# Kernel tuning notes

Hardware: AMD Instinct MI355X
Metric: run time of the kernel (lower is better)

## Reference

```python
import jax, jax.numpy as jnp
import numpy as np

# ---- fixed problem dims (match init_kwargs) ----
B = 256            # graph pairs
NQ, NC = 96, 120   # nodes per query / corpus graph
EQ, EC = 192, 240  # edges per query / corpus graph
M = 256            # max_edge_set_size (pad target)
RAW = 32           # raw node/edge feature dim
H = 64             # node_state_dim
MSG = 128          # message_dim == encoded edge dim
SDIM = 64          # sinkhorn_feature_dim
PROP_STEPS = 3
TIME_STEPS = 2
SINK_ITERS = 10
TEMP = 0.1
N_NODES = B * (NQ + NC)
N_EDGES = B * (EQ + EC)


def _mlp2(x, W1, b1, W2, b2):
    return jax.nn.relu(x @ W1 + b1) @ W2 + b2


def _split_and_stack(ef):
    # edges laid out [q0, c0, q1, c1, ...]; pad each graph's edges to M
    D = ef.shape[-1]
    ef = ef.reshape(B, EQ + EC, D)
    q = jnp.pad(ef[:, :EQ], ((0, 0), (0, M - EQ), (0, 0)))
    c = jnp.pad(ef[:, EQ:], ((0, 0), (0, M - EC), (0, 0)))
    return q, c


def _sinkhorn(log_alpha):
    la = log_alpha / TEMP
    for _ in range(SINK_ITERS):
        la = la - jax.nn.logsumexp(la, axis=2, keepdims=True)
        la = la - jax.nn.logsumexp(la, axis=1, keepdims=True)
    return jnp.exp(la)


def setup_inputs() -> dict:
    key = jax.random.key(0)
    ks = jax.random.split(key, 16)
    rng = np.random.default_rng(0)
    nodes_per_graph = np.tile(np.array([NQ, NC]), B)            # [2B]
    node_offsets = np.concatenate([[0], np.cumsum(nodes_per_graph)[:-1]])
    edges_per_graph = np.tile(np.array([EQ, EC]), B)
    eg = np.repeat(np.arange(2 * B), edges_per_graph)           # graph id per edge
    from_idx = node_offsets[eg] + rng.integers(0, nodes_per_graph[eg])
    to_idx = node_offsets[eg] + rng.integers(0, nodes_per_graph[eg])

    def lin(k, i, o):
        return (jax.random.normal(k, (i, o), jnp.float32) / np.sqrt(i)).astype(jnp.float32)

    return {
        "node_features": jax.random.normal(ks[0], (N_NODES, RAW), jnp.float32),
        "edge_features": jax.random.normal(ks[1], (N_EDGES, RAW), jnp.float32),
        "from_idx": jnp.asarray(from_idx, jnp.int32),
        "to_idx": jnp.asarray(to_idx, jnp.int32),
        "enc_node_W": lin(ks[2], RAW, H), "enc_node_b": jnp.zeros((H,), jnp.float32),
        "enc_edge_W": lin(ks[3], RAW, MSG), "enc_edge_b": jnp.zeros((MSG,), jnp.float32),
        "msg_W1": lin(ks[4], 2 * H + MSG, 2 * MSG), "msg_b1": jnp.zeros((2 * MSG,), jnp.float32),
        "msg_W2": lin(ks[5], 2 * MSG, MSG), "msg_b2": jnp.zeros((MSG,), jnp.float32),
        "upd_W1": lin(ks[6], H + 2 * MSG, 2 * H), "upd_b1": jnp.zeros((2 * H,), jnp.float32),
        "upd_W2": lin(ks[7], 2 * H, H), "upd_b2": jnp.zeros((H,), jnp.float32),
        "int_W1": lin(ks[8], 2 * MSG, 2 * MSG), "int_b1": jnp.zeros((2 * MSG,), jnp.float32),
        "int_W2": lin(ks[9], 2 * MSG, MSG), "int_b2": jnp.zeros((MSG,), jnp.float32),
        "sink_W1": lin(ks[10], MSG, SDIM), "sink_b1": jnp.zeros((SDIM,), jnp.float32),
        "sink_W2": lin(ks[11], SDIM, SDIM), "sink_b2": jnp.zeros((SDIM,), jnp.float32),
    }


def _forward(node_features, edge_features,
             enc_node_W, enc_node_b, enc_edge_W, enc_edge_b,
             msg_W1, msg_b1, msg_W2, msg_b2,
             upd_W1, upd_b1, upd_W2, upd_b2,
             int_W1, int_b1, int_W2, int_b2,
             sink_W1, sink_b1, sink_W2, sink_b2,
             from_idx, to_idx):
    h0 = node_features @ enc_node_W + enc_node_b      # GraphEncoder (nodes)
    e0 = edge_features @ enc_edge_W + enc_edge_b      # GraphEncoder (edges) -> MSG dim
    mask_q = (jnp.arange(M) < EQ).astype(h0.dtype)[None, :, None]
    mask_c = (jnp.arange(M) < EC).astype(h0.dtype)[None, :, None]

    def edge_msgs(h, comb):
        hf, ht = h[from_idx], h[to_idx]
        mf = _mlp2(jnp.concatenate([hf, ht, comb], -1), msg_W1, msg_b1, msg_W2, msg_b2)
        mb = _mlp2(jnp.concatenate([ht, hf, comb], -1), msg_W1, msg_b1, msg_W2, msg_b2)
        return mf, mb

    plan = None
    q_store = c_store = None
    for _ in range(TIME_STEPS):
        h, e = h0, e0
        inter = jnp.zeros((N_EDGES, MSG), e0.dtype)
        for _ in range(PROP_STEPS):
            # interaction encoder on [edge_features_enc, interaction_features]
            comb = _mlp2(jnp.concatenate([e, inter], -1), int_W1, int_b1, int_W2, int_b2)
            # prop_layer: bidirectional messages + aggregation + node update
            mf, mb = edge_msgs(h, comb)
            agg_f = jax.ops.segment_sum(mf, to_idx, num_segments=N_NODES)
            agg_b = jax.ops.segment_sum(mb, from_idx, num_segments=N_NODES)
            h = _mlp2(jnp.concatenate([h, agg_f, agg_b], -1), upd_W1, upd_b1, upd_W2, upd_b2)
            # propagation_messages: per-edge messages from updated node states
            mf2, mb2 = edge_msgs(h, comb)
            e = mf2 + mb2
            # interaction features via transport-plan gather (zeros on first time step)
            if plan is None:
                inter = jnp.zeros((N_EDGES, MSG), e.dtype)
            else:
                qs, cs = _split_and_stack(e)
                q_int = jnp.einsum('bqc,bcd->bqd', plan, cs)[:, :EQ]
                c_int = jnp.einsum('bqc,bqd->bcd', plan, qs)[:, :EC]
                inter = jnp.concatenate([q_int, c_int], 1).reshape(N_EDGES, MSG)
        q_store, c_store = _split_and_stack(e)
        fq = _mlp2(q_store, sink_W1, sink_b1, sink_W2, sink_b2) * mask_q
        fc = _mlp2(c_store, sink_W1, sink_b1, sink_W2, sink_b2) * mask_c
        plan = _sinkhorn(jnp.einsum('bqd,bcd->bqc', fq, fc))
    # feature_alignment_score: -||Q - P C||_1 per pair
    return -jnp.abs(q_store - jnp.einsum('bqc,bcd->bqd', plan, c_store)).sum((1, 2))


def reference(node_features, edge_features, from_idx, to_idx,
              enc_node_W, enc_node_b, enc_edge_W, enc_edge_b,
              msg_W1, msg_b1, msg_W2, msg_b2,
              upd_W1, upd_b1, upd_W2, upd_b2,
              int_W1, int_b1, int_W2, int_b2,
              sink_W1, sink_b1, sink_W2, sink_b2):
    return _forward(node_features, edge_features,
                    enc_node_W, enc_node_b, enc_edge_W, enc_edge_b,
                    msg_W1, msg_b1, msg_W2, msg_b2,
                    upd_W1, upd_b1, upd_W2, upd_b2,
                    int_W1, int_b1, int_W2, int_b2,
                    sink_W1, sink_b1, sink_W2, sink_b2,
                    from_idx, to_idx)
```

## Files before the change

### kernel.cpp

```cpp
#include <hip/hip_runtime.h>
#include <math.h>

constexpr int BATCH = 256;
constexpr int EQ_   = 192;
constexpr int EC_   = 240;
constexpr int EPG   = 432;
constexpr int NPG   = 216;
constexpr int NN    = BATCH * NPG;
constexpr int NE    = BATCH * EPG;

typedef __attribute__((ext_vector_type(8))) short short8;
typedef __attribute__((ext_vector_type(4))) float floatx4;
typedef unsigned short u16;

__device__ __forceinline__ u16 f2bf(float x) {
  union { float f; unsigned u; } c; c.f = x;
  const unsigned r = (c.u + 0x7FFFu + ((c.u >> 16) & 1u)) >> 16;
  return (u16)r;
}
__device__ __forceinline__ float bf2f(u16 x) {
  union { unsigned u; float f; } c; c.u = ((unsigned)x) << 16;
  return c.f;
}
__device__ __forceinline__ unsigned pack2(float a, float b) {
  return (unsigned)f2bf(a) | ((unsigned)f2bf(b) << 16);
}
__device__ __forceinline__ short8 cvt8(const float* __restrict__ p) {
  const float4 a = *(const float4*)p;
  const float4 b = *(const float4*)(p + 4);
  short8 o;
  o[0]=(short)f2bf(a.x); o[1]=(short)f2bf(a.y); o[2]=(short)f2bf(a.z); o[3]=(short)f2bf(a.w);
  o[4]=(short)f2bf(b.x); o[5]=(short)f2bf(b.y); o[6]=(short)f2bf(b.z); o[7]=(short)f2bf(b.w);
  return o;
}

__device__ __forceinline__ void lse_online(float& m, float& s, float tt) {
  if (tt > m) { s = s * __expf(m - tt) + 1.f; m = tt; }
  else        { s += __expf(tt - m); }
}

__global__ __launch_bounds__(256)
void wconv(const float* __restrict__ W, u16* __restrict__ out, int K, int N)
{
  const int i = blockIdx.x * 256 + threadIdx.x;
  if (i < K * N) {
    const int n = i / K, k = i - n * K;
    out[i] = f2bf(W[(size_t)k * N + n]);
  }
}

template<int K1, int HID, int NOUT, int IN_MODE, int DUAL, int OUT_MODE, int WAVES>
__global__ __launch_bounds__(WAVES * 64, 4)
void mlp_mfma(const void* __restrict__ X, const void* __restrict__ P2,
              const void* __restrict__ P3, const u16* __restrict__ CB,
              const int* __restrict__ IA, const int* __restrict__ IB,
              const u16* __restrict__ W1t, const float* __restrict__ B1,
              const u16* __restrict__ W2t, const float* __restrict__ B2,
              float* __restrict__ Yf, u16* __restrict__ Yb0, u16* __restrict__ Yb1)
{
  constexpr int RT  = 32;
  constexpr int THREADS = WAVES * 64;
  constexpr int KCH = K1 / 8;
  constexpr int NT1 = HID / (WAVES * 16);
  constexpr int NT2 = (NOUT / (WAVES * 16) > 0) ? NOUT / (WAVES * 16) : 1;
  constexpr int SAB = RT * K1 * 2;
  constexpr int SHB = RT * (HID + 8) * 2;
  __shared__ __align__(16) char smem[(SAB > SHB ? SAB : SHB)];
  u16* sA = (u16*)smem;
  u16* sH = (u16*)smem;

  const int tid = threadIdx.x;
  const int rowBase = blockIdx.x * RT;

  for (int ch = tid; ch < RT * KCH; ch += THREADS) {
    const int r = ch / KCH, kc = ch - r * KCH;
    const int gr = rowBase + r, k0 = kc * 8;
    short8 pk;
    if constexpr (IN_MODE == 4) {
      const float* Xf  = (const float*)X;
      const float* P2f = (const float*)P2;
      if (k0 < 128)      pk = cvt8(&Xf[(size_t)gr * 128 + k0]);
      else if (P2f)      pk = cvt8(&P2f[(size_t)gr * 128 + (k0 - 128)]);
      else { pk = short8{0,0,0,0,0,0,0,0}; }
    } else if constexpr (IN_MODE == 1) {
      const u16* Hb = (const u16*)X;
      if (k0 < 64)       pk = *(const short8*)&Hb[(size_t)IA[gr] * 64 + k0];
      else if (k0 < 128) pk = *(const short8*)&Hb[(size_t)IB[gr] * 64 + (k0 - 64)];
      else               pk = *(const short8*)&CB[(size_t)gr * 128 + (k0 - 128)];
    } else {
      const u16* Hb = (const u16*)X;
      const u16* A0 = (const u16*)P2;
      const u16* A1 = (const u16*)P3;
      if (k0 < 64)       pk = *(const short8*)&Hb[(size_t)gr * 64 + k0];
      else if (k0 < 192) pk = *(const short8*)&A0[(size_t)gr * 128 + (k0 - 64)];
      else               pk = *(const short8*)&A1[(size_t)gr * 128 + (k0 - 192)];
    }
    const int byte = ((r * K1 + k0) * 2) ^ ((r & 7) << 4);
    *(short8*)((char*)sA + byte) = pk;
  }
  __syncthreads();

  const int wid = tid >> 6, lane = tid & 63;
  const int l15 = lane & 15, lg = lane >> 4;

  floatx4 acc1[1 + DUAL][2][NT1];
  #pragma unroll
  for (int d = 0; d <= DUAL; ++d)
    #pragma unroll
    for (int m = 0; m < 2; ++m)
      #pragma unroll
      for (int n = 0; n < NT1; ++n) acc1[d][m][n] = floatx4{0.f,0.f,0.f,0.f};

  #pragma unroll 2
  for (int kk = 0; kk < K1 / 32; ++kk) {
    short8 bw[NT1];
    #pragma unroll
    for (int n = 0; n < NT1; ++n) {
      const int col = wid * (HID / WAVES) + n * 16 + l15;
      bw[n] = *(const short8*)&W1t[(size_t)col * K1 + kk * 32 + lg * 8];
    }
    #pragma unroll
    for (int d = 0; d <= DUAL; ++d) {
      int k0 = kk * 32 + lg * 8;
      if (DUAL && d && k0 < 128) k0 ^= 64;
      #pragma unroll
      for (int m = 0; m < 2; ++m) {
        const int r = m * 16 + l15;
        const int byte = ((r * K1 + k0) * 2) ^ ((r & 7) << 4);
        const short8 af = *(const short8*)((char*)sA + byte);
        #pragma unroll
        for (int n = 0; n < NT1; ++n)
          acc1[d][m][n] = __builtin_amdgcn_mfma_f32_16x16x32_bf16(af, bw[n], acc1[d][m][n], 0, 0, 0);
      }
    }
  }
  __syncthreads();

  floatx4 accO[2][NT2];
  #pragma unroll
  for (int m = 0; m < 2; ++m)
    #pragma unroll
    for (int n = 0; n < NT2; ++n) accO[m][n] = floatx4{0.f,0.f,0.f,0.f};

  #pragma unroll
  for (int d = 0; d <= DUAL; ++d) {
    #pragma unroll
    for (int n = 0; n < NT1; ++n) {
      const int col = wid * (HID / WAVES) + n * 16 + l15;
      const float b1 = B1[col];
      #pragma unroll
      for (int m = 0; m < 2; ++m)
        #pragma unroll
        for (int r = 0; r < 4; ++r) {
          const int row = m * 16 + lg * 4 + r;
          const float y = acc1[d][m][n][r] + b1;
          sH[row * (HID + 8) + col] = f2bf(y > 0.f ? y : 0.f);
        }
    }
    __syncthreads();
    if (OUT_MODE == 2 && d == 1) {
      #pragma unroll
      for (int m = 0; m < 2; ++m)
        #pragma unroll
        for (int n = 0; n < NT2; ++n) accO[m][n] = floatx4{0.f,0.f,0.f,0.f};
    }
    #pragma unroll 2
    for (int kk = 0; kk < HID / 32; ++kk) {
      short8 bw2[NT2];
      #pragma unroll
      for (int n = 0; n < NT2; ++n) {
        const int col = wid * (NOUT / WAVES) + n * 16 + l15;
        bw2[n] = *(const short8*)&W2t[(size_t)col * HID + kk * 32 + lg * 8];
      }
      #pragma unroll
      for (int m = 0; m < 2; ++m) {
        const short8 af = *(const short8*)&sH[(m * 16 + l15) * (HID + 8) + kk * 32 + lg * 8];
        #pragma unroll
        for (int n = 0; n < NT2; ++n)
          accO[m][n] = __builtin_amdgcn_mfma_f32_16x16x32_bf16(af, bw2[n], accO[m][n], 0, 0, 0);
      }
    }
    if constexpr (OUT_MODE == 2) {
      u16* Y = d ? Yb1 : Yb0;
      #pragma unroll
      for (int n = 0; n < NT2; ++n) {
        const int col = wid * (NOUT / WAVES) + n * 16 + l15;
        const float b2 = B2[col];
        #pragma unroll
        for (int m = 0; m < 2; ++m)
          #pragma unroll
          for (int r = 0; r < 4; ++r) {
            const int gr = rowBase + m * 16 + lg * 4 + r;
            Y[(size_t)gr * NOUT + col] = f2bf(accO[m][n][r] + b2);
          }
      }
    }
    if (DUAL && d == 0) __syncthreads();
  }

  if constexpr (OUT_MODE != 2) {
    #pragma unroll
    for (int n = 0; n < NT2; ++n) {
      const int col = wid * (NOUT / WAVES) + n * 16 + l15;
      const float b2 = B2[col] * (float)(1 + DUAL);
      #pragma unroll
      for (int m = 0; m < 2; ++m)
        #pragma unroll
        for (int r = 0; r < 4; ++r) {
          const int gr = rowBase + m * 16 + lg * 4 + r;
          const float y = accO[m][n][r] + b2;
          if constexpr (OUT_MODE == 1) Yb0[(size_t)gr * NOUT + col] = f2bf(y);
          else                         Yf[(size_t)gr * NOUT + col] = y;
        }
    }
  }
}

__global__ __launch_bounds__(512)
void scatter_agg(const u16* __restrict__ MF, const u16* __restrict__ MB,
                 const int* __restrict__ FI, const int* __restrict__ TI,
                 u16* __restrict__ AggF, u16* __restrict__ AggB)
{
  const int pair = blockIdx.x >> 1, dir = blockIdx.x & 1;
  const u16* M  = dir ? MB : MF;
  const int* SI = dir ? FI : TI;
  u16* Agg      = dir ? AggB : AggF;
  const int tid = threadIdx.x;
  __shared__ float sAgg[NPG * 128];

  for (int i = tid; i < NPG * 128; i += 512) sAgg[i] = 0.f;
  __syncthreads();

  for (int i = tid; i < EPG * 32; i += 512) {
    const int edge = i >> 5, cb = i & 31;
    const int er = pair * EPG + edge;
    const int node = SI[er] - pair * NPG;
    const size_t base = (size_t)er * 128 + cb;
    #pragma unroll
    for (int k = 0; k < 4; ++k)
      atomicAdd(&sAgg[node * 128 + cb + 32 * k], bf2f(M[base + 32 * k]));
  }
  __syncthreads();
  unsigned* dst = (unsigned*)(Agg + (size_t)pair * NPG * 128);
  for (int i = tid; i < NPG * 64; i += 512)
    dst[i] = pack2(sAgg[2 * i], sAgg[2 * i + 1]);
}

template<int K1, int HID, int NOUT, int IN_MODE, int SINGLE, int OUTBF>
__global__ __launch_bounds__(256)
void fused_mlp(const float* __restrict__ X, const float* __restrict__ P1,
               const float* __restrict__ W1, const float* __restrict__ B1,
               const float* __restrict__ W2, const float* __restrict__ B2,
               float* __restrict__ Y, u16* __restrict__ Yb, int maskLen)
{
  constexpr int RT = 32, BK = 32;
  constexpr int J1 = HID / 32;
  constexpr int J2 = NOUT / 32;
  constexpr int BMAX = (HID > NOUT ? HID : NOUT);
  __shared__ float sA[RT * 33];
  __shared__ float sB[BK * BMAX];
  __shared__ float sH[SINGLE ? 1 : RT * (HID + 1)];

  const int t  = threadIdx.x;
  const int tx = t & 31, ty = t >> 5;
  const int rowBase = blockIdx.x * RT;

  float acc[4][J1];
  #pragma unroll
  for (int i = 0; i < 4; ++i)
    #pragma unroll
    for (int j = 0; j < J1; ++j) acc[i][j] = 0.f;

  for (int kb = 0; kb < K1; kb += BK) {
    for (int l = t; l < RT * BK; l += 256) {
      const int r = l >> 5, k = l & 31;
      const int gr = rowBase + r, gk = kb + k;
      float v;
      if constexpr (IN_MODE == 0) {
        v = X[(size_t)gr * K1 + gk];
      } else {
        const int bb = gr >> 8, m = gr & 255;
        constexpr int off = (IN_MODE == 5) ? 0 : EQ_;
        constexpr int len = (IN_MODE == 5) ? EQ_ : EC_;
        v = (m < len) ? P1[((size_t)bb * EPG + off + m) * 128 + gk] : 0.f;
      }
      sA[r * 33 + k] = v;
    }
    for (int l = t * 4; l < BK * HID; l += 1024) {
      *(float4*)&sB[l] = *(const float4*)&W1[(size_t)(kb + l / HID) * HID + (l % HID)];
    }
    __syncthreads();
    #pragma unroll
    for (int k = 0; k < BK; ++k) {
      const float a0 = sA[(ty*4+0)*33+k], a1 = sA[(ty*4+1)*33+k],
                  a2 = sA[(ty*4+2)*33+k], a3 = sA[(ty*4+3)*33+k];
      #pragma unroll
      for (int j = 0; j < J1; ++j) {
        const float bb = sB[k * HID + tx + 32*j];
        acc[0][j] += a0 * bb; acc[1][j] += a1 * bb;
        acc[2][j] += a2 * bb; acc[3][j] += a3 * bb;
      }
    }
    __syncthreads();
  }

  if constexpr (SINGLE) {
    #pragma unroll
    for (int j = 0; j < J1; ++j) {
      const int col = tx + 32*j;
      const float bias = B1[col];
      #pragma unroll
      for (int i = 0; i < 4; ++i) {
        const int gr = rowBase + ty*4 + i;
        if constexpr (OUTBF) Yb[(size_t)gr * HID + col] = f2bf(acc[i][j] + bias);
        else                 Y[(size_t)gr * HID + col] = acc[i][j] + bias;
      }
    }
  } else {
    #pragma unroll
    for (int j = 0; j < J1; ++j) {
      const int col = tx + 32*j;
      const float bias = B1[col];
      #pragma unroll
      for (int i = 0; i < 4; ++i) {
        float y = acc[i][j] + bias;
        sH[(ty*4+i) * (HID+1) + col] = y > 0.f ? y : 0.f;
      }
    }
    __syncthreads();

    float acc2[4][J2];
    #pragma unroll
    for (int i = 0; i < 4; ++i)
      #pragma unroll
      for (int j = 0; j < J2; ++j) acc2[i][j] = 0.f;

    for (int kb = 0; kb < HID; kb += BK) {
      for (int l = t * 4; l < BK * NOUT; l += 1024) {
        *(float4*)&sB[l] = *(const float4*)&W2[(size_t)(kb + l / NOUT) * NOUT + (l % NOUT)];
      }
      __syncthreads();
      #pragma unroll
      for (int k = 0; k < BK; ++k) {
        const float a0 = sH[(ty*4+0)*(HID+1) + kb + k],
                    a1 = sH[(ty*4+1)*(HID+1) + kb + k],
                    a2 = sH[(ty*4+2)*(HID+1) + kb + k],
                    a3 = sH[(ty*4+3)*(HID+1) + kb + k];
        #pragma unroll
        for (int j = 0; j < J2; ++j) {
          const float bb = sB[k * NOUT + tx + 32*j];
          acc2[0][j] += a0 * bb; acc2[1][j] += a1 * bb;
          acc2[2][j] += a2 * bb; acc2[3][j] += a3 * bb;
        }
      }
      __syncthreads();
    }
    #pragma unroll
    for (int j = 0; j < J2; ++j) {
      const int col = tx + 32*j;
      const float bias = B2[col];
      #pragma unroll
      for (int i = 0; i < 4; ++i) {
        const int gr = rowBase + ty*4 + i;
        float y = acc2[i][j] + bias;
        if (maskLen >= 0 && (gr & 255) >= maskLen) y = 0.f;
        Y[(size_t)gr * NOUT + col] = y;
      }
    }
  }
}

__global__ __launch_bounds__(256)
void gemm_nt_scale(const float* __restrict__ A, const float* __restrict__ Bm,
                   float* __restrict__ C, float scale)
{
  const int b = blockIdx.z, qt = blockIdx.x, ct = blockIdx.y;
  __shared__ float sA[64 * 68];
  __shared__ float sB[64 * 68];
  const int t = threadIdx.x;
  const int tx = t & 15, ty = t >> 4;
  const float* Ab = A  + (size_t)b * 16384 + (size_t)qt * 4096;
  const float* Bb = Bm + (size_t)b * 16384 + (size_t)ct * 4096;
  for (int l = t * 4; l < 64 * 64; l += 1024) {
    const int r = l >> 6, d = l & 63;
    *(float4*)&sA[r*68 + d] = *(const float4*)&Ab[r*64 + d];
    *(float4*)&sB[r*68 + d] = *(const float4*)&Bb[r*64 + d];
  }
  __syncthreads();
  float acc[4][4] = {};
  #pragma unroll
  for (int d = 0; d < 64; ++d) {
    float a[4], bb[4];
    #pragma unroll
    for (int i = 0; i < 4; ++i) a[i]  = sA[(ty*4+i)*68 + d];
    #pragma unroll
    for (int j = 0; j < 4; ++j) bb[j] = sB[(tx+16*j)*68 + d];
    #pragma unroll
    for (int i = 0; i < 4; ++i)
      #pragma unroll
      for (int j = 0; j < 4; ++j) acc[i][j] += a[i] * bb[j];
  }
  float* Cb = C + (size_t)b * 65536 + (size_t)(qt*64) * 256 + ct*64;
  #pragma unroll
  for (int i = 0; i < 4; ++i)
    #pragma unroll
    for (int j = 0; j < 4; ++j)
      Cb[(ty*4+i)*256 + tx + 16*j] = acc[i][j] * scale;
}

template<int TRANSA>
__global__ __launch_bounds__(256)
void gemm_plan_mfma(const float* __restrict__ P, const float* __restrict__ E,
                    float* __restrict__ Y, int RPB, int YOFF, int VOFF,
                    int VLEN, int maskRows)
{
  __shared__ u16 sP[64 * 40];
  __shared__ u16 sVT[128 * 40];
  const int b = blockIdx.y, rt = blockIdx.x;
  const int t = threadIdx.x;
  const int wid = t >> 6, lane = t & 63;
  const int l15 = lane & 15, lg = lane >> 4;
  const float* Pb = P + (size_t)b * 65536;

  floatx4 acc[8];
  #pragma unroll
  for (int n = 0; n < 8; ++n) acc[n] = floatx4{0.f,0.f,0.f,0.f};

  for (int kb = 0; kb < 256; kb += 32) {
    if constexpr (TRANSA == 0) {
      for (int l = t; l < 64 * 32; l += 256) {
        const int r = l >> 5, k = l & 31;
        sP[r * 40 + k] = f2bf(Pb[(size_t)(rt * 64 + r) * 256 + kb + k]);
      }
    } else {
      for (int l = t; l < 64 * 32; l += 256) {
        const int q = l >> 6, c = l & 63;
        sP[c * 40 + q] = f2bf(Pb[(size_t)(kb + q) * 256 + rt * 64 + c]);
      }
    }
    for (int l = t; l < 32 * 128; l += 256) {
      const int k = l >> 7, d = l & 127;
      const int vr = kb + k;
      float v = 0.f;
      if (vr < VLEN) v = E[((size_t)b * EPG + VOFF + vr) * 128 + d];
      sVT[d * 40 + k] = f2bf(v);
    }
    __syncthreads();
    const short8 af = *(const short8*)&sP[(wid * 16 + l15) * 40 + lg * 8];
    #pragma unroll
    for (int n = 0; n < 8; ++n) {
      const short8 bw = *(const short8*)&sVT[(n * 16 + l15) * 40 + lg * 8];
      acc[n] = __builtin_amdgcn_mfma_f32_16x16x32_bf16(af, bw, acc[n], 0, 0, 0);
    }
    __syncthreads();
  }
  #pragma unroll
  for (int n = 0; n < 8; ++n) {
    const int col = n * 16 + l15;
    #pragma unroll
    for (int r = 0; r < 4; ++r) {
      const int row = rt * 64 + wid * 16 + lg * 4 + r;
      if (row < maskRows)
        Y[((size_t)b * RPB + YOFF + row) * 128 + col] = acc[n][r];
    }
  }
}

__global__ __launch_bounds__(1024)
void sinkhorn_fused(float* __restrict__ S)
{
  const int b = blockIdx.x, t = threadIdx.x;
  float* Sb = S + (size_t)b * 65536;
  const int w = t >> 6, lane = t & 63;
  const int cbase = lane * 4;
  __shared__ float pm[16 * 256], ps[16 * 256];
  __shared__ float su[256], sv[256];
  if (t < 256) sv[t] = 0.f;
  __syncthreads();

  for (int it = 0; it < 10; ++it) {
    const float4 v4 = *(const float4*)&sv[cbase];
    float4 cm = {-1e30f, -1e30f, -1e30f, -1e30f};
    float4 cs = {0.f, 0.f, 0.f, 0.f};
    #pragma unroll 2
    for (int i = 0; i < 16; ++i) {
      const int r = w * 16 + i;
      const float4 s4 = *(const float4*)&Sb[(size_t)r * 256 + cbase];
      const float ax = s4.x + v4.x, ay = s4.y + v4.y;
      const float az = s4.z + v4.z, aw = s4.w + v4.w;
      float m = fmaxf(fmaxf(ax, ay), fmaxf(az, aw));
      #pragma unroll
      for (int off = 32; off; off >>= 1) m = fmaxf(m, __shfl_xor(m, off));
      float s = __expf(ax - m) + __expf(ay - m) + __expf(az - m) + __expf(aw - m);
      #pragma unroll
      for (int off = 32; off; off >>= 1) s += __shfl_xor(s, off);
      const float u = -(m + __logf(s));
      if (lane == 0) su[r] = u;
      lse_online(cm.x, cs.x, s4.x + u);
      lse_online(cm.y, cs.y, s4.y + u);
      lse_online(cm.z, cs.z, s4.z + u);
      lse_online(cm.w, cs.w, s4.w + u);
    }
    *(float4*)&pm[w * 256 + cbase] = cm;
    *(float4*)&ps[w * 256 + cbase] = cs;
    __syncthreads();
    if (t < 256) {
      float m = pm[t];
      #pragma unroll
      for (int k = 1; k < 16; ++k) m = fmaxf(m, pm[k * 256 + t]);
      float s = 0.f;
      #pragma unroll
      for (int k = 0; k < 16; ++k) s += ps[k * 256 + t] * __expf(pm[k * 256 + t] - m);
      sv[t] = -(m + __logf(s));
    }
    __syncthreads();
  }
  for (int i = t; i < 16384; i += 1024) {
    const int row = i >> 6, c4 = (i & 63) * 4;
    float4 s4 = *(float4*)&Sb[(size_t)row * 256 + c4];
    const float uu = su[row];
    const float4 v4 = *(const float4*)&sv[c4];
    s4.x = __expf(s4.x + uu + v4.x);
    s4.y = __expf(s4.y + uu + v4.y);
    s4.z = __expf(s4.z + uu + v4.z);
    s4.w = __expf(s4.w + uu + v4.w);
    *(float4*)&Sb[(size_t)row * 256 + c4] = s4;
  }
}

__global__ __launch_bounds__(256)
void escore_kernel(const float* __restrict__ e, const float* __restrict__ pc,
                   float* __restrict__ out)
{
  const int b = blockIdx.x, t = threadIdx.x;
  float acc = 0.f;
  for (int i4 = t; i4 < 8192; i4 += 256) {
    const int flat = i4 * 4;
    const int m = flat >> 7, d = flat & 127;
    float4 p = *(const float4*)&pc[((size_t)b * 256 + m) * 128 + d];
    float4 q = {0.f, 0.f, 0.f, 0.f};
    if (m < EQ_) q = *(const float4*)&e[((size_t)b * EPG + m) * 128 + d];
    acc += fabsf(q.x - p.x) + fabsf(q.y - p.y) + fabsf(q.z - p.z) + fabsf(q.w - p.w);
  }
  __shared__ float red[256];
  red[t] = acc; __syncthreads();
  for (int s2 = 128; s2 > 0; s2 >>= 1) { if (t < s2) red[t] += red[t + s2]; __syncthreads(); }
  if (t == 0) out[b] = -red[0];
}

extern "C" void kernel_launch(void* const* d_in, const int* in_sizes, int n_in,
                              void* d_out, int out_size, void* d_ws, size_t ws_size,
                              hipStream_t stream)
{
  const float* node_features = (const float*)d_in[0];
  const float* edge_features = (const float*)d_in[1];
  const int*   from_idx      = (const int*)d_in[2];
  const int*   to_idx        = (const int*)d_in[3];
  const float* enc_node_W = (const float*)d_in[4];
  const float* enc_node_b = (const float*)d_in[5];
  const float* enc_edge_W = (const float*)d_in[6];
  const float* enc_edge_b = (const float*)d_in[7];
  const float* msg_W1 = (const float*)d_in[8];
  const float* msg_b1 = (const float*)d_in[9];
  const float* msg_W2 = (const float*)d_in[10];
  const float* msg_b2 = (const float*)d_in[11];
  const float* upd_W1 = (const float*)d_in[12];
  const float* upd_b1 = (const float*)d_in[13];
  const float* upd_W2 = (const float*)d_in[14];
  const float* upd_b2 = (const float*)d_in[15];
  const float* int_W1 = (const float*)d_in[16];
  const float* int_b1 = (const float*)d_in[17];
  const float* int_W2 = (const float*)d_in[18];
  const float* int_b2 = (const float*)d_in[19];
  const float* sink_W1 = (const float*)d_in[20];
  const float* sink_b1 = (const float*)d_in[21];
  const float* sink_W2 = (const float*)d_in[22];
  const float* sink_b2 = (const float*)d_in[23];
  float* out = (float*)d_out;

  float* wsf = (float*)d_ws;
  float* hreg = wsf;
  float* e   = hreg + (size_t)NN * 64;
  float* shr = e + (size_t)NE * 128;
  float* S   = shr + (size_t)NE * 128;
  u16* comb  = (u16*)(S + (size_t)BATCH * 65536);
  u16* wi1 = comb + (size_t)NE * 128;
  u16* wi2 = wi1 + 65536;
  u16* wm1 = wi2 + 32768;
  u16* wm2 = wm1 + 65536;
  u16* wu1 = wm2 + 32768;
  u16* wu2 = wu1 + 40960;

  u16* hb  = (u16*)hreg;
  u16* mfb = (u16*)e;
  u16* mbb = mfb + (size_t)NE * 128;

  u16* aggFb = (u16*)shr;
  u16* aggBb = aggFb + (size_t)NN * 128;
  float* inter = shr;
  float* fq    = shr;
  float* fc    = shr + (size_t)BATCH * 16384;

  wconv<<<256, 256, 0, stream>>>(int_W1, wi1, 256, 256);
  wconv<<<128, 256, 0, stream>>>(int_W2, wi2, 256, 128);
  wconv<<<256, 256, 0, stream>>>(msg_W1, wm1, 256, 256);
  wconv<<<128, 256, 0, stream>>>(msg_W2, wm2, 256, 128);
  wconv<<<160, 256, 0, stream>>>(upd_W1, wu1, 320, 128);
  wconv<<< 32, 256, 0, stream>>>(upd_W2, wu2, 128, 64);

  for (int ts = 0; ts < 2; ++ts) {
    fused_mlp<32,64,64,0,1,1><<<NN/32, 256, 0, stream>>>(
        node_features, nullptr, enc_node_W, enc_node_b, nullptr, nullptr,
        nullptr, hb, -1);
    fused_mlp<32,128,128,0,1,0><<<NE/32, 256, 0, stream>>>(
        edge_features, nullptr, enc_edge_W, enc_edge_b, nullptr, nullptr,
        e, nullptr, -1);

    for (int p = 0; p < 3; ++p) {
      const float* interArg = (ts == 1 && p > 0) ? inter : nullptr;
      mlp_mfma<256,256,128,4,0,1,8><<<NE/32, 512, 0, stream>>>(
          e, interArg, nullptr, nullptr, nullptr, nullptr,
          wi1, int_b1, wi2, int_b2, nullptr, comb, nullptr);
      mlp_mfma<256,256,128,1,1,2,8><<<NE/32, 512, 0, stream>>>(
          hb, nullptr, nullptr, comb, from_idx, to_idx,
          wm1, msg_b1, wm2, msg_b2, nullptr, mfb, mbb);
      scatter_agg<<<BATCH*2, 512, 0, stream>>>(mfb, mbb, from_idx, to_idx, aggFb, aggBb);
      mlp_mfma<320,128,64,3,0,1,4><<<NN/32, 256, 0, stream>>>(
          hb, aggFb, aggBb, nullptr, nullptr, nullptr,
          wu1, upd_b1, wu2, upd_b2, nullptr, hb, nullptr);
      mlp_mfma<256,256,128,1,1,0,8><<<NE/32, 512, 0, stream>>>(
          hb, nullptr, nullptr, comb, from_idx, to_idx,
          wm1, msg_b1, wm2, msg_b2, e, nullptr, nullptr);
      if (ts == 1 && p < 2) {
        gemm_plan_mfma<0><<<dim3(4, BATCH), 256, 0, stream>>>(
            S, e, inter, EPG, 0,   EQ_, EC_, EQ_);
        gemm_plan_mfma<1><<<dim3(4, BATCH), 256, 0, stream>>>(
            S, e, inter, EPG, EQ_, 0,   EQ_, EC_);
      }
    }
    fused_mlp<128,64,64,5,0,0><<<BATCH*8, 256, 0, stream>>>(
        nullptr, e, sink_W1, sink_b1, sink_W2, sink_b2, fq, nullptr, EQ_);
    fused_mlp<128,64,64,6,0,0><<<BATCH*8, 256, 0, stream>>>(
        nullptr, e, sink_W1, sink_b1, sink_W2, sink_b2, fc, nullptr, EC_);
    gemm_nt_scale<<<dim3(4,4,BATCH), 256, 0, stream>>>(fq, fc, S, 10.0f);
    sinkhorn_fused<<<BATCH, 1024, 0, stream>>>(S);
  }

  gemm_plan_mfma<0><<<dim3(4, BATCH), 256, 0, stream>>>(S, e, shr, 256, 0, EQ_, EC_, 256);
  escore_kernel<<<BATCH, 256, 0, stream>>>(e, shr, out);
}
```

Baseline: 4.036 ms.

## Fuse interaction MLP and bidirectional message MLP into one kernel

Replaces two launches, the interaction MLP that writes comb and the message MLP that reads it back and gathers node states, with a single kernel. The comb tile stays in shared memory and is reused as input to both message directions, and the forward and backward messages go into one interleaved buffer. The scatter kernel now reads from that interleaved layout. This removes a global round trip of comb and one launch, at the cost of more barriers and a serialized per-block pipeline with 4-block occupancy hints.

Result: no change. 4.000 ms (-0.9%).

```diff
diff --git a/kernel.cpp b/kernel.cpp
--- a/kernel.cpp
+++ b/kernel.cpp
@@ -216,13 +216,192 @@
   }
 }
 
+__global__ __launch_bounds__(512, 4)
+void comb_msg_fused(const float* __restrict__ E, const float* __restrict__ INTER,
+                    const u16* __restrict__ Hb,
+                    const int* __restrict__ IA, const int* __restrict__ IB,
+                    const u16* __restrict__ Wi1, const float* __restrict__ Bi1,
+                    const u16* __restrict__ Wi2, const float* __restrict__ Bi2,
+                    const u16* __restrict__ Wm1, const float* __restrict__ Bm1,
+                    const u16* __restrict__ Wm2, const float* __restrict__ Bm2,
+                    u16* __restrict__ COMB, u16* __restrict__ MI )
+{
+  constexpr int RT = 32;
+  __shared__ __align__(16) char smem[RT * (256 + 8) * 2];
+  u16* sA = (u16*)smem;
+  u16* sH = (u16*)smem;
+
+  const int tid = threadIdx.x;
+  const int rowBase = blockIdx.x * RT;
+  const int wid = tid >> 6, lane = tid & 63;
+  const int l15 = lane & 15, lg = lane >> 4;
+
+  for (int ch = tid; ch < RT * 32; ch += 512) {
+    const int r = ch >> 5, kc = ch & 31;
+    const int gr = rowBase + r, k0 = kc * 8;
+    short8 pk;
+    if (k0 < 128)   pk = cvt8(&E[(size_t)gr * 128 + k0]);
+    else if (INTER) pk = cvt8(&INTER[(size_t)gr * 128 + (k0 - 128)]);
+    else            pk = short8{0,0,0,0,0,0,0,0};
+    const int byte = ((r * 256 + k0) * 2) ^ ((r & 7) << 4);
+    *(short8*)((char*)sA + byte) = pk;
+  }
+  __syncthreads();
+
+  floatx4 c1[2][2];
+  #pragma unroll
+  for (int m = 0; m < 2; ++m) { c1[m][0] = floatx4{0,0,0,0}; c1[m][1] = floatx4{0,0,0,0}; }
+  #pragma unroll 2
+  for (int kk = 0; kk < 8; ++kk) {
+    short8 bw[2];
+    #pragma unroll
+    for (int n = 0; n < 2; ++n) {
+      const int col = wid * 32 + n * 16 + l15;
+      bw[n] = *(const short8*)&Wi1[(size_t)col * 256 + kk * 32 + lg * 8];
+    }
+    #pragma unroll
+    for (int m = 0; m < 2; ++m) {
+      const int r = m * 16 + l15;
+      const int byte = ((r * 256 + kk * 32 + lg * 8) * 2) ^ ((r & 7) << 4);
+      const short8 af = *(const short8*)((char*)sA + byte);
+      c1[m][0] = __builtin_amdgcn_mfma_f32_16x16x32_bf16(af, bw[0], c1[m][0], 0, 0, 0);
+      c1[m][1] = __builtin_amdgcn_mfma_f32_16x16x32_bf16(af, bw[1], c1[m][1], 0, 0, 0);
+    }
+  }
+  __syncthreads();
+  #pragma unroll
+  for (int n = 0; n < 2; ++n) {
+    const int col = wid * 32 + n * 16 + l15;
+    const float b1 = Bi1[col];
+    #pragma unroll
+    for (int m = 0; m < 2; ++m)
+      #pragma unroll
+      for (int r = 0; r < 4; ++r) {
+        const int row = m * 16 + lg * 4 + r;
+        const float y = c1[m][n][r] + b1;
+        sH[row * 264 + col] = f2bf(y > 0.f ? y : 0.f);
+      }
+  }
+  __syncthreads();
+  floatx4 cO[2];
+  cO[0] = floatx4{0,0,0,0}; cO[1] = floatx4{0,0,0,0};
+  #pragma unroll 2
+  for (int kk = 0; kk < 8; ++kk) {
+    const int col = wid * 16 + l15;
+    const short8 bw2 = *(const short8*)&Wi2[(size_t)col * 256 + kk * 32 + lg * 8];
+    #pragma unroll
+    for (int m = 0; m < 2; ++m) {
+      const short8 af = *(const short8*)&sH[(m * 16 + l15) * 264 + kk * 32 + lg * 8];
+      cO[m] = __builtin_amdgcn_mfma_f32_16x16x32_bf16(af, bw2, cO[m], 0, 0, 0);
+    }
+  }
+  __syncthreads();
+
+  {
+    const int col = wid * 16 + l15;
+    const float b2 = Bi2[col];
+    #pragma unroll
+    for (int m = 0; m < 2; ++m)
+      #pragma unroll
+      for (int r = 0; r < 4; ++r) {
+        const int row = m * 16 + lg * 4 + r;
+        const int gr = rowBase + row;
+        const u16 v = f2bf(cO[m][r] + b2);
+        COMB[(size_t)gr * 128 + col] = v;
+        const int k0 = 128 + col;
+        const int byte = ((row * 256 + k0) * 2) ^ ((row & 7) << 4);
+        *(u16*)((char*)sA + byte) = v;
+      }
+  }
+  for (int ch = tid; ch < RT * 16; ch += 512) {
+    const int r = ch >> 4, kc = ch & 15;
+    const int gr = rowBase + r, k0 = kc * 8;
+    short8 pk;
+    if (k0 < 64) pk = *(const short8*)&Hb[(size_t)IA[gr] * 64 + k0];
+    else         pk = *(const short8*)&Hb[(size_t)IB[gr] * 64 + (k0 - 64)];
+    const int byte = ((r * 256 + k0) * 2) ^ ((r & 7) << 4);
+    *(short8*)((char*)sA + byte) = pk;
+  }
+  __syncthreads();
+
+  floatx4 m1[2][2][2];
+  #pragma unroll
+  for (int d = 0; d < 2; ++d)
+    #pragma unroll
+    for (int m = 0; m < 2; ++m) { m1[d][m][0] = floatx4{0,0,0,0}; m1[d][m][1] = floatx4{0,0,0,0}; }
+  #pragma unroll 2
+  for (int kk = 0; kk < 8; ++kk) {
+    short8 bw[2];
+    #pragma unroll
+    for (int n = 0; n < 2; ++n) {
+      const int col = wid * 32 + n * 16 + l15;
+      bw[n] = *(const short8*)&Wm1[(size_t)col * 256 + kk * 32 + lg * 8];
+    }
+    #pragma unroll
+    for (int d = 0; d < 2; ++d) {
+      int k0 = kk * 32 + lg * 8;
+      if (d && k0 < 128) k0 ^= 64;
+      #pragma unroll
+      for (int m = 0; m < 2; ++m) {
+        const int r = m * 16 + l15;
+        const int byte = ((r * 256 + k0) * 2) ^ ((r & 7) << 4);
+        const short8 af = *(const short8*)((char*)sA + byte);
+        m1[d][m][0] = __builtin_amdgcn_mfma_f32_16x16x32_bf16(af, bw[0], m1[d][m][0], 0, 0, 0);
+        m1[d][m][1] = __builtin_amdgcn_mfma_f32_16x16x32_bf16(af, bw[1], m1[d][m][1], 0, 0, 0);
+      }
+    }
+  }
+  __syncthreads();
+
+  floatx4 mO[2];
+  #pragma unroll
+  for (int d = 0; d < 2; ++d) {
+    #pragma unroll
+    for (int n = 0; n < 2; ++n) {
+      const int col = wid * 32 + n * 16 + l15;
+      const float b1 = Bm1[col];
+      #pragma unroll
+      for (int m = 0; m < 2; ++m)
+        #pragma unroll
+        for (int r = 0; r < 4; ++r) {
+          const int row = m * 16 + lg * 4 + r;
+          const float y = m1[d][m][n][r] + b1;
+          sH[row * 264 + col] = f2bf(y > 0.f ? y : 0.f);
+        }
+    }
+    __syncthreads();
+    mO[0] = floatx4{0,0,0,0}; mO[1] = floatx4{0,0,0,0};
+    #pragma unroll 2
+    for (int kk = 0; kk < 8; ++kk) {
+      const int col = wid * 16 + l15;
+      const short8 bw2 = *(const short8*)&Wm2[(size_t)col * 256 + kk * 32 + lg * 8];
+      #pragma unroll
+      for (int m = 0; m < 2; ++m) {
+        const short8 af = *(const short8*)&sH[(m * 16 + l15) * 264 + kk * 32 + lg * 8];
+        mO[m] = __builtin_amdgcn_mfma_f32_16x16x32_bf16(af, bw2, mO[m], 0, 0, 0);
+      }
+    }
+    {
+      const int col = wid * 16 + l15;
+      const float b2 = Bm2[col];
+      #pragma unroll
+      for (int m = 0; m < 2; ++m)
+        #pragma unroll
+        for (int r = 0; r < 4; ++r) {
+          const int gr = rowBase + m * 16 + lg * 4 + r;
+          MI[(size_t)gr * 256 + d * 128 + col] = f2bf(mO[m][r] + b2);
+        }
+    }
+    if (d == 0) __syncthreads();
+  }
+}
+
 __global__ __launch_bounds__(512)
-void scatter_agg(const u16* __restrict__ MF, const u16* __restrict__ MB,
+void scatter_agg(const u16* __restrict__ MI,
                  const int* __restrict__ FI, const int* __restrict__ TI,
                  u16* __restrict__ AggF, u16* __restrict__ AggB)
 {
   const int pair = blockIdx.x >> 1, dir = blockIdx.x & 1;
-  const u16* M  = dir ? MB : MF;
   const int* SI = dir ? FI : TI;
   u16* Agg      = dir ? AggB : AggF;
   const int tid = threadIdx.x;
@@ -235,10 +414,10 @@
     const int edge = i >> 5, cb = i & 31;
     const int er = pair * EPG + edge;
     const int node = SI[er] - pair * NPG;
-    const size_t base = (size_t)er * 128 + cb;
+    const size_t base = (size_t)er * 256 + dir * 128 + cb;
     #pragma unroll
     for (int k = 0; k < 4; ++k)
-      atomicAdd(&sAgg[node * 128 + cb + 32 * k], bf2f(M[base + 32 * k]));
+      atomicAdd(&sAgg[node * 128 + cb + 32 * k], bf2f(MI[base + 32 * k]));
   }
   __syncthreads();
   unsigned* dst = (unsigned*)(Agg + (size_t)pair * NPG * 128);
@@ -591,9 +770,8 @@
   u16* wu1 = wm2 + 32768;
   u16* wu2 = wu1 + 40960;
 
-  u16* hb  = (u16*)hreg;
-  u16* mfb = (u16*)e;
-  u16* mbb = mfb + (size_t)NE * 128;
+  u16* hb = (u16*)hreg;
+  u16* mI = (u16*)e;
 
   u16* aggFb = (u16*)shr;
   u16* aggBb = aggFb + (size_t)NN * 128;
@@ -618,13 +796,11 @@
 
     for (int p = 0; p < 3; ++p) {
       const float* interArg = (ts == 1 && p > 0) ? inter : nullptr;
-      mlp_mfma<256,256,128,4,0,1,8><<<NE/32, 512, 0, stream>>>(
-          e, interArg, nullptr, nullptr, nullptr, nullptr,
-          wi1, int_b1, wi2, int_b2, nullptr, comb, nullptr);
-      mlp_mfma<256,256,128,1,1,2,8><<<NE/32, 512, 0, stream>>>(
-          hb, nullptr, nullptr, comb, from_idx, to_idx,
-          wm1, msg_b1, wm2, msg_b2, nullptr, mfb, mbb);
-      scatter_agg<<<BATCH*2, 512, 0, stream>>>(mfb, mbb, from_idx, to_idx, aggFb, aggBb);
+      comb_msg_fused<<<NE/32, 512, 0, stream>>>(
+          e, interArg, hb, from_idx, to_idx,
+          wi1, int_b1, wi2, int_b2, wm1, msg_b1, wm2, msg_b2,
+          comb, mI);
+      scatter_agg<<<BATCH*2, 512, 0, stream>>>(mI, from_idx, to_idx, aggFb, aggBb);
       mlp_mfma<320,128,64,3,0,1,4><<<NN/32, 256, 0, stream>>>(
           hb, aggFb, aggBb, nullptr, nullptr, nullptr,
           wu1, upd_b1, wu2, upd_b2, nullptr, hb, nullptr);
```
